# Performance work log

Measured on AMD Instinct MI355X. Metric: run time of the kernel, lower is better.

Reference implementation:

```python
import jax, jax.numpy as jnp
import numpy as np
import math

NUM_HEADS = 8
DIM_Q = 512
DIM_K = 512
DIM_V = 512
EPS = 1e-5


def _layernorm(x, g, b):
    mu = jnp.mean(x, axis=-1, keepdims=True)
    var = jnp.mean(jnp.square(x - mu), axis=-1, keepdims=True)
    return (x - mu) * jax.lax.rsqrt(var + EPS) * g + b


def setup_inputs() -> dict:
    key = jax.random.key(0)
    ks = jax.random.split(key, 16)
    B, Nq, Nk = 8, 1024, 1024
    s_q = 1.0 / math.sqrt(DIM_Q)
    s_v = 1.0 / math.sqrt(DIM_V)
    return {
        "Q": jax.random.normal(ks[0], (B, Nq, DIM_Q), jnp.float32),
        "K": jax.random.normal(ks[1], (B, Nk, DIM_K), jnp.float32),
        "Wq": jax.random.uniform(ks[2], (DIM_Q, DIM_V), jnp.float32, -s_q, s_q),
        "bq": jax.random.uniform(ks[3], (DIM_V,), jnp.float32, -s_q, s_q),
        "Wk": jax.random.uniform(ks[4], (DIM_K, DIM_V), jnp.float32, -s_q, s_q),
        "bk": jax.random.uniform(ks[5], (DIM_V,), jnp.float32, -s_q, s_q),
        "Wv": jax.random.uniform(ks[6], (DIM_K, DIM_V), jnp.float32, -s_q, s_q),
        "bv": jax.random.uniform(ks[7], (DIM_V,), jnp.float32, -s_q, s_q),
        "Wo": jax.random.uniform(ks[8], (DIM_V, DIM_V), jnp.float32, -s_v, s_v),
        "bo": jax.random.uniform(ks[9], (DIM_V,), jnp.float32, -s_v, s_v),
        "g0": jnp.ones((DIM_V,), jnp.float32),
        "b0": jnp.zeros((DIM_V,), jnp.float32),
        "g1": jnp.ones((DIM_V,), jnp.float32),
        "b1": jnp.zeros((DIM_V,), jnp.float32),
        "M": jax.random.randint(ks[10], (B, Nq, Nk), 0, 2, jnp.int32),
    }


def reference(Q, K, Wq, bq, Wk, bk, Wv, bv, Wo, bo, g0, b0, g1, b1, M):
    B, Nq, _ = Q.shape
    Nk = K.shape[1]
    H = NUM_HEADS
    d = DIM_V // H
    # projections
    Qp = Q @ Wq + bq                      # [B,Nq,Dv]
    Kp = K @ Wk + bk                      # [B,Nk,Dv]
    Vp = K @ Wv + bv                      # [B,Nk,Dv]
    # split heads: channel h*d+j -> head h (matches torch split/cat ordering)
    Qh = Qp.reshape(B, Nq, H, d)
    Kh = Kp.reshape(B, Nk, H, d)
    Vh = Vp.reshape(B, Nk, H, d)
    # scores scaled by sqrt(dim_V) (faithful to original, NOT sqrt(head_dim))
    A = jnp.einsum("bqhd,bkhd->bhqk", Qh, Kh) / math.sqrt(DIM_V)
    A = jnp.where(M[:, None, :, :] == 0, -jnp.inf, A)
    A = jax.nn.softmax(A, axis=-1)
    # residual add of the (projected, per-head) query, then merge heads
    O = Qh + jnp.einsum("bhqk,bkhd->bqhd", A, Vh)
    O = O.reshape(B, Nq, DIM_V)
    O = _layernorm(O, g0, b0)
    O = O + jax.nn.relu(O @ Wo + bo)
    O = _layernorm(O, g1, b1)
    return O
```

## Files before the change

### kernel.cpp

```cpp
#include <hip/hip_runtime.h>

typedef unsigned short u16;
typedef unsigned int u32;
typedef unsigned long long u64;
typedef __attribute__((ext_vector_type(8))) short short8;
typedef __attribute__((ext_vector_type(4))) float f32x4;
typedef __attribute__((ext_vector_type(4))) u32 u32x4;

#define BATCH 8
#define NSEQ 1024
#define DMODEL 512
#define HDIM 64
#define SCALE_LOG2E 0.06375871114929199f
#define FIXED_MAX 16.0f

#define O_QBF 0ULL
#define O_KBF 8388608ULL
#define O_WB  16777216ULL
#define O_MB  18874368ULL
#define O_QP  19922944ULL
#define O_KP  28311552ULL
#define O_VP  36700160ULL

__device__ __forceinline__ u16 f2bf(float f) {
  u32 u = __float_as_uint(f);
  u = (u + 0x7fffu + ((u >> 16) & 1u)) >> 16;
  return (u16)u;
}
__device__ __forceinline__ float bf2f(u16 s) {
  return __uint_as_float(((u32)s) << 16);
}
__device__ __forceinline__ void gload16(const void* g, void* l) {
  __builtin_amdgcn_global_load_lds((const __attribute__((address_space(1))) void*)g,
                                   (__attribute__((address_space(3))) void*)l, 16, 0, 0);
}
__device__ __forceinline__ u32 cvtpk(float a, float b) {
  u32 r;
  asm("v_cvt_pk_bf16_f32 %0, %1, %2" : "=v"(r) : "v"(a), "v"(b));
  return r;
}

__global__ __launch_bounds__(256) void prep_kernel(
    const float* __restrict__ Wq, const float* __restrict__ Wk,
    const float* __restrict__ Wv, const float* __restrict__ Wo,
    const int* __restrict__ M,
    u16* __restrict__ Wb, u64* __restrict__ Mb)
{
  __shared__ float lds[64 * 68];
  const int bi = blockIdx.x, t = threadIdx.x;
  if (bi < 256) {
    const int w = bi >> 6;
    const int tt = bi & 63;
    const int tr = tt >> 3, tc = tt & 7;
    const float* W = (w == 0) ? Wq : (w == 1) ? Wk : (w == 2) ? Wv : Wo;
#pragma unroll
    for (int j = 0; j < 4; ++j) {
      int vi = j * 256 + t;
      int row = vi >> 4, c4 = vi & 15;
      float4 v = *(const float4*)(W + (size_t)(tr * 64 + row) * 512 + tc * 64 + c4 * 4);
      lds[row * 68 + c4 * 4 + 0] = v.x;
      lds[row * 68 + c4 * 4 + 1] = v.y;
      lds[row * 68 + c4 * 4 + 2] = v.z;
      lds[row * 68 + c4 * 4 + 3] = v.w;
    }
    __syncthreads();
#pragma unroll
    for (int j = 0; j < 2; ++j) {
      int oi = j * 256 + t;
      int nl = oi >> 3, k8 = oi & 7;
      short8 o;
#pragma unroll
      for (int i = 0; i < 8; ++i) o[i] = (short)f2bf(lds[(k8 * 8 + i) * 68 + nl]);
      *(short8*)(Wb + (size_t)w * 262144 + (size_t)(tc * 64 + nl) * 512 + tr * 64 + k8 * 8) = o;
    }
  } else {
    const int pb = bi - 256;
    const int wv = t >> 6, lane = t & 63;
    for (int i = 0; i < 32; ++i) {
      int widx = pb * 128 + wv * 32 + i;
      int kc = widx & 15;
      int qq = (widx >> 4) & 1023;
      int bb = widx >> 14;
      int mv = M[((size_t)bb * 1024 + qq) * 1024 + kc * 64 + lane];
      u64 bal = __ballot(mv != 0);
      if (lane == 0) Mb[widx] = bal;
    }
  }
}

template<int MODE>
__global__ __launch_bounds__(256) void gemm_bt(
    const float* __restrict__ Fq, const float* __restrict__ Fk,
    const u16* __restrict__ Abf,
    const u16* __restrict__ Wb,
    const float* __restrict__ b0, const float* __restrict__ b1, const float* __restrict__ b2,
    u16* __restrict__ outp, const u16* __restrict__ resid)
{
  __shared__ __align__(16) char Alds[8192];
  __shared__ __align__(16) char Blds[8192];
  const int tid = threadIdx.x;
  const int wv = tid >> 6, lane = tid & 63;
  const int g16 = lane >> 4, l16 = lane & 15;
  const int wr = wv >> 1, wc = wv & 1;

  const int p = blockIdx.x;
  const int xcd = p & 7, rest = p >> 3;
  const int bx = xcd + ((rest & 7) << 3);
  const int q2 = rest >> 3;
  const int by = (MODE == 0) ? (q2 & 3) : q2;
  const int bz = (MODE == 0) ? (q2 >> 2) : 0;

  const float* Af; const u16* A; const u16* W; const float* bias; u16* out;
  if (MODE == 0) {
    Af = (bz == 0) ? Fq : Fk;
    A = nullptr;
    W = Wb + (size_t)bz * 262144;
    bias = (bz == 0) ? b0 : ((bz == 1) ? b1 : b2);
    out = outp + (size_t)bz * 4194304;
  } else {
    Af = nullptr; A = Abf; W = Wb; bias = b0; out = outp;
  }

  const int m0 = bx * 128, n0 = by * 128;
  f32x4 acc[4][4] = {};

  for (int kt = 0; kt < 16; ++kt) {
    const int k0 = kt * 32;
#pragma unroll
    for (int r = 0; r < 2; ++r) {
      int idx = r * 256 + tid;
      int row = idx >> 2, sl = idx & 3;
      if (MODE == 0) {
        const float* ap = Af + (size_t)(m0 + row) * 512 + k0 + sl * 8;
        float4 a0 = *(const float4*)(ap);
        float4 a1 = *(const float4*)(ap + 4);
        u32x4 wpk;
        wpk[0] = cvtpk(a0.x, a0.y);
        wpk[1] = cvtpk(a0.z, a0.w);
        wpk[2] = cvtpk(a1.x, a1.y);
        wpk[3] = cvtpk(a1.z, a1.w);
        *(u32x4*)(Alds + (size_t)idx * 16) = wpk;
      } else {
        gload16(A + (size_t)(m0 + row) * 512 + k0 + sl * 8, Alds + r * 4096 + wv * 1024);
      }
      gload16(W + (size_t)(n0 + row) * 512 + k0 + sl * 8, Blds + r * 4096 + wv * 1024);
    }
    __syncthreads();
    short8 af[4], bfr[4];
#pragma unroll
    for (int mt = 0; mt < 4; ++mt)
      af[mt] = *(const short8*)(Alds + (wr * 64 + mt * 16 + l16) * 64 + g16 * 16);
#pragma unroll
    for (int nt = 0; nt < 4; ++nt)
      bfr[nt] = *(const short8*)(Blds + (wc * 64 + nt * 16 + l16) * 64 + g16 * 16);
#pragma unroll
    for (int mt = 0; mt < 4; ++mt)
#pragma unroll
      for (int nt = 0; nt < 4; ++nt)
        acc[mt][nt] = __builtin_amdgcn_mfma_f32_16x16x32_bf16(af[mt], bfr[nt], acc[mt][nt], 0, 0, 0);
    __syncthreads();
  }

#pragma unroll
  for (int nt = 0; nt < 4; ++nt) {
    int col = n0 + wc * 64 + nt * 16 + l16;
    float bcol = bias[col];
#pragma unroll
    for (int mt = 0; mt < 4; ++mt) {
#pragma unroll
      for (int r = 0; r < 4; ++r) {
        int row = m0 + wr * 64 + mt * 16 + g16 * 4 + r;
        float v = acc[mt][nt][r] + bcol;
        if (MODE == 1) {
          v = fmaxf(v, 0.f) + bf2f(resid[(size_t)row * 512 + col]);
        }
        out[(size_t)row * 512 + col] = f2bf(v);
      }
    }
  }
}

__global__ __launch_bounds__(256, 4) void attn_kernel(
    const u16* __restrict__ Qp, const u16* __restrict__ Kp, const u16* __restrict__ Vp,
    const u64* __restrict__ Mb, u16* __restrict__ O1)
{
  __shared__ __align__(16) char K_lds[2][8192];
  __shared__ __align__(16) char VT_lds[2][8192];

  const int tid = threadIdx.x;
  const int wv = tid >> 6, lane = tid & 63;
  const int g16 = lane >> 4, l16 = lane & 15;
  const int l7 = l16 & 7;

  const int wg = blockIdx.x;
  const int swz = (wg & 7) * 128 + (wg >> 3);
  const int qt = swz & 15;
  const int h = (swz >> 4) & 7;
  const int b = swz >> 7;
  const int qg = qt * 64;
  const int hb = h * HDIM;
  const size_t batch_row = (size_t)b * NSEQ;

  const int q = qg + wv * 16 + l16;
  const int dv2 = (tid & 31) * 2;
  const int kg = tid >> 5;
  const int v_kc = kg >> 2, v_gg = kg & 3;

  short8 b_q[2];
#pragma unroll
  for (int c = 0; c < 2; ++c) {
    short8 raw = *(const short8*)(Qp + (batch_row + q) * DMODEL + hb + c * 32 + g16 * 8);
    short8 sc;
#pragma unroll
    for (int j = 0; j < 8; ++j) sc[j] = (short)f2bf(bf2f((u16)raw[j]) * SCALE_LOG2E);
    b_q[c] = sc;
  }

  const u64* Mq = Mb + (batch_row + q) * 16;

  auto stageK = [&](int kt2, char* dst) {
#pragma unroll
    for (int r = 0; r < 2; ++r) {
      int idx = r * 256 + tid;
      int row = idx >> 3, sl = idx & 7;
      int chunk = sl ^ (row & 7);
      gload16(Kp + (batch_row + kt2 * 64 + row) * DMODEL + hb + chunk * 8,
              dst + r * 4096 + wv * 1024);
    }
  };
  auto loadV = [&](int kt2, u32 (&vr)[8]) {
#pragma unroll
    for (int j = 0; j < 8; ++j) {
      int row = v_kc * 32 + (j >> 2) * 16 + v_gg * 4 + (j & 3);
      vr[j] = *(const u32*)(Vp + (batch_row + kt2 * 64 + row) * DMODEL + hb + dv2);
    }
  };
  auto writeVT = [&](const u32 (&vr)[8], char* dstv) {
    u32x4 lo, hi;
#pragma unroll
    for (int i = 0; i < 4; ++i) {
      lo[i] = __builtin_amdgcn_perm(vr[2 * i + 1], vr[2 * i], 0x05040100u);
      hi[i] = __builtin_amdgcn_perm(vr[2 * i + 1], vr[2 * i], 0x07060302u);
    }
    *(u32x4*)(dstv + dv2 * 128 + ((kg ^ (dv2 & 7)) << 4)) = lo;
    *(u32x4*)(dstv + (dv2 + 1) * 128 + ((kg ^ ((dv2 + 1) & 7)) << 4)) = hi;
  };

  float lL = 0.f;
  f32x4 accO[4] = {};

  u32 vreg[8];
  u64 mksA, mksB;

  stageK(0, &K_lds[0][0]);
  loadV(0, vreg);
  mksA = Mq[0];
  writeVT(vreg, &VT_lds[0][0]);
  loadV(1, vreg);

#define ATTN_TILE(KT, CUR, MKS, MKSN)                                          \
  do {                                                                         \
    asm volatile("s_waitcnt vmcnt(8) lgkmcnt(0)" ::: "memory");                \
    __builtin_amdgcn_sched_barrier(0);                                         \
    __builtin_amdgcn_s_barrier();                                              \
    __builtin_amdgcn_sched_barrier(0);                                         \
    char* Kc = &K_lds[CUR][0];                                                 \
    char* Vc = &VT_lds[CUR][0];                                                \
    if ((KT) < 15) {                                                           \
      writeVT(vreg, &VT_lds[(CUR) ^ 1][0]);                                    \
      stageK((KT) + 1, &K_lds[(CUR) ^ 1][0]);                                  \
      loadV((KT) + 2 < 16 ? (KT) + 2 : 15, vreg);                              \
      MKSN = Mq[(KT) + 1];                                                     \
    }                                                                          \
    f32x4 s_[4];                                                               \
    __builtin_amdgcn_s_setprio(1);                                             \
    _Pragma("unroll")                                                          \
    for (int kf = 0; kf < 4; ++kf) {                                           \
      int row = kf * 16 + l16;                                                 \
      short8 ak0 = *(const short8*)(Kc + row * 128 + ((g16 ^ l7) << 4));       \
      short8 ak1 = *(const short8*)(Kc + row * 128 + (((4 + g16) ^ l7) << 4)); \
      u32 nib = ((u32)((MKS) >> (kf * 16 + g16 * 4))) & 15u;                   \
      f32x4 acc;                                                               \
      acc[0] = (nib & 1u) ? 0.f : -32768.f;                                    \
      acc[1] = (nib & 2u) ? 0.f : -32768.f;                                    \
      acc[2] = (nib & 4u) ? 0.f : -32768.f;                                    \
      acc[3] = (nib & 8u) ? 0.f : -32768.f;                                    \
      acc = __builtin_amdgcn_mfma_f32_16x16x32_bf16(ak0, b_q[0], acc, 0, 0, 0);\
      acc = __builtin_amdgcn_mfma_f32_16x16x32_bf16(ak1, b_q[1], acc, 0, 0, 0);\
      s_[kf] = acc;                                                            \
    }                                                                          \
    __builtin_amdgcn_s_setprio(0);                                             \
    float sum = 0.f;                                                           \
    u32 c0a[4], c1a[4];                                                        \
    _Pragma("unroll")                                                          \
    for (int kf = 0; kf < 4; ++kf) {                                           \
      float e0 = __builtin_amdgcn_exp2f(s_[kf][0] - FIXED_MAX);                \
      float e1 = __builtin_amdgcn_exp2f(s_[kf][1] - FIXED_MAX);                \
      float e2 = __builtin_amdgcn_exp2f(s_[kf][2] - FIXED_MAX);                \
      float e3 = __builtin_amdgcn_exp2f(s_[kf][3] - FIXED_MAX);                \
      sum += (e0 + e1) + (e2 + e3);                                            \
      c0a[kf] = cvtpk(e0, e1);                                                 \
      c1a[kf] = cvtpk(e2, e3);                                                 \
    }                                                                          \
    lL += sum;                                                                 \
    u32x4 t0 = {c0a[0], c1a[0], c0a[1], c1a[1]};                               \
    u32x4 t1 = {c0a[2], c1a[2], c0a[3], c1a[3]};                               \
    short8 b_p0 = *(short8*)&t0;                                               \
    short8 b_p1 = *(short8*)&t1;                                               \
    __builtin_amdgcn_s_setprio(1);                                             \
    _Pragma("unroll")                                                          \
    for (int f = 0; f < 4; ++f) {                                              \
      int vrow = f * 16 + l16;                                                 \
      short8 av0 = *(const short8*)(Vc + vrow * 128 + ((g16 ^ l7) << 4));      \
      short8 av1 = *(const short8*)(Vc + vrow * 128 + (((4 + g16) ^ l7) << 4));\
      accO[f] = __builtin_amdgcn_mfma_f32_16x16x32_bf16(av0, b_p0, accO[f], 0, 0, 0); \
      accO[f] = __builtin_amdgcn_mfma_f32_16x16x32_bf16(av1, b_p1, accO[f], 0, 0, 0); \
    }                                                                          \
    __builtin_amdgcn_s_setprio(0);                                             \
  } while (0)

  for (int t = 0; t < 8; ++t) {
    ATTN_TILE(2 * t, 0, mksA, mksB);
    ATTN_TILE(2 * t + 1, 1, mksB, mksA);
  }
#undef ATTN_TILE

  float l = lL;
  l += __shfl_xor(l, 16, 64);
  l += __shfl_xor(l, 32, 64);
  float inv = 1.0f / fmaxf(l, 1e-20f);
#pragma unroll
  for (int f = 0; f < 4; ++f) {
    size_t o = (batch_row + q) * DMODEL + hb + f * 16 + g16 * 4;
    u64 qh = *(const u64*)(Qp + o);
    u64 ov = 0;
#pragma unroll
    for (int r = 0; r < 4; ++r) {
      float val = accO[f][r] * inv + bf2f((u16)(qh >> (r * 16)));
      ov |= ((u64)f2bf(val)) << (r * 16);
    }
    *(u64*)(O1 + o) = ov;
  }
}

template<int OUTF>
__global__ __launch_bounds__(256) void ln_kernel(
    const u16* __restrict__ X, const float* __restrict__ g, const float* __restrict__ bb,
    void* __restrict__ outv)
{
  const int tid = threadIdx.x;
  const int wv = tid >> 6, lane = tid & 63;
  const size_t row = (size_t)blockIdx.x * 4 + wv;
  short8 x8 = *(const short8*)(X + row * 512 + lane * 8);
  float xf[8];
  float s = 0.f, s2 = 0.f;
#pragma unroll
  for (int i = 0; i < 8; ++i) {
    xf[i] = bf2f((u16)x8[i]);
    s += xf[i];
    s2 += xf[i] * xf[i];
  }
#pragma unroll
  for (int d = 1; d < 64; d <<= 1) {
    s += __shfl_xor(s, d, 64);
    s2 += __shfl_xor(s2, d, 64);
  }
  float mu = s * (1.f / 512.f);
  float var = s2 * (1.f / 512.f) - mu * mu;
  float rs = rsqrtf(var + 1e-5f);
  float4 ga = *(const float4*)(g + lane * 8);
  float4 gb = *(const float4*)(g + lane * 8 + 4);
  float4 ba = *(const float4*)(bb + lane * 8);
  float4 bc = *(const float4*)(bb + lane * 8 + 4);
  float gv[8] = {ga.x, ga.y, ga.z, ga.w, gb.x, gb.y, gb.z, gb.w};
  float bv[8] = {ba.x, ba.y, ba.z, ba.w, bc.x, bc.y, bc.z, bc.w};
  float y[8];
#pragma unroll
  for (int i = 0; i < 8; ++i) y[i] = (xf[i] - mu) * rs * gv[i] + bv[i];
  if (OUTF) {
    float* o = (float*)outv + row * 512 + lane * 8;
    float4 o1 = {y[0], y[1], y[2], y[3]};
    float4 o2 = {y[4], y[5], y[6], y[7]};
    *(float4*)o = o1;
    *(float4*)(o + 4) = o2;
  } else {
    short8 o;
#pragma unroll
    for (int i = 0; i < 8; ++i) o[i] = (short)f2bf(y[i]);
    *(short8*)((u16*)outv + row * 512 + lane * 8) = o;
  }
}

extern "C" void kernel_launch(void* const* d_in, const int* in_sizes, int n_in,
                              void* d_out, int out_size, void* d_ws, size_t ws_size,
                              hipStream_t stream) {
  (void)in_sizes; (void)n_in; (void)out_size; (void)ws_size;
  const float* Q  = (const float*)d_in[0];
  const float* K  = (const float*)d_in[1];
  const float* Wq = (const float*)d_in[2];
  const float* bq = (const float*)d_in[3];
  const float* Wk = (const float*)d_in[4];
  const float* bk = (const float*)d_in[5];
  const float* Wv = (const float*)d_in[6];
  const float* bv = (const float*)d_in[7];
  const float* Wo = (const float*)d_in[8];
  const float* bo = (const float*)d_in[9];
  const float* g0 = (const float*)d_in[10];
  const float* b0 = (const float*)d_in[11];
  const float* g1 = (const float*)d_in[12];
  const float* b1 = (const float*)d_in[13];
  const int*   M  = (const int*)d_in[14];
  float* out = (float*)d_out;
  char* ws = (char*)d_ws;

  u16* Wb  = (u16*)(ws + O_WB);
  u64* Mb  = (u64*)(ws + O_MB);
  u16* Qp  = (u16*)(ws + O_QP);
  u16* Kp  = (u16*)(ws + O_KP);
  u16* Vp  = (u16*)(ws + O_VP);
  u16* O1  = (u16*)(ws + O_QBF);
  u16* Xn  = Qp;
  u16* Z   = (u16*)(ws + O_KBF);

  prep_kernel<<<1280, 256, 0, stream>>>(Wq, Wk, Wv, Wo, M, Wb, Mb);
  gemm_bt<0><<<768, 256, 0, stream>>>(Q, K, nullptr, Wb, bq, bk, bv, Qp, nullptr);
  attn_kernel<<<1024, 256, 0, stream>>>(Qp, Kp, Vp, Mb, O1);
  ln_kernel<0><<<2048, 256, 0, stream>>>(O1, g0, b0, (void*)Xn);
  gemm_bt<1><<<256, 256, 0, stream>>>(nullptr, nullptr, Xn, Wb + 3 * 262144, bo,
                                      nullptr, nullptr, Z, Xn);
  ln_kernel<1><<<2048, 256, 0, stream>>>(Z, g1, b1, (void*)out);
}
```

Before: 116.5 us.

## Move mask bit-packing into projection GEMM launch and software-pipeline fp32 A loads

The mask ballot-packing work moves out of the prep kernel into extra blocks of the QKV projection GEMM launch, so the prep kernel shrinks to weight conversion and the mask pass can run alongside the GEMM tiles. The MODE 0 GEMM now software-pipelines its main loop: fp32 A tiles are prefetched into registers two steps ahead, and W tiles are staged via async LDS loads, with explicit waitcnt and barriers. This is meant to hide global load latency behind the MFMA work and shorten the prep kernel's critical path. In exchange it adds register pressure and hand-placed synchronisation, and the mask blocks now compete with GEMM blocks for CUs.

```diff
diff --git a/kernel.cpp b/kernel.cpp
--- a/kernel.cpp
+++ b/kernel.cpp
@@ -43,41 +43,55 @@
 __global__ __launch_bounds__(256) void prep_kernel(
     const float* __restrict__ Wq, const float* __restrict__ Wk,
     const float* __restrict__ Wv, const float* __restrict__ Wo,
-    const int* __restrict__ M,
-    u16* __restrict__ Wb, u64* __restrict__ Mb)
+    u16* __restrict__ Wb)
 {
   __shared__ float lds[64 * 68];
   const int bi = blockIdx.x, t = threadIdx.x;
-  if (bi < 256) {
-    const int w = bi >> 6;
-    const int tt = bi & 63;
-    const int tr = tt >> 3, tc = tt & 7;
-    const float* W = (w == 0) ? Wq : (w == 1) ? Wk : (w == 2) ? Wv : Wo;
-#pragma unroll
-    for (int j = 0; j < 4; ++j) {
-      int vi = j * 256 + t;
-      int row = vi >> 4, c4 = vi & 15;
-      float4 v = *(const float4*)(W + (size_t)(tr * 64 + row) * 512 + tc * 64 + c4 * 4);
-      lds[row * 68 + c4 * 4 + 0] = v.x;
-      lds[row * 68 + c4 * 4 + 1] = v.y;
-      lds[row * 68 + c4 * 4 + 2] = v.z;
-      lds[row * 68 + c4 * 4 + 3] = v.w;
-    }
-    __syncthreads();
-#pragma unroll
-    for (int j = 0; j < 2; ++j) {
-      int oi = j * 256 + t;
-      int nl = oi >> 3, k8 = oi & 7;
-      short8 o;
-#pragma unroll
-      for (int i = 0; i < 8; ++i) o[i] = (short)f2bf(lds[(k8 * 8 + i) * 68 + nl]);
-      *(short8*)(Wb + (size_t)w * 262144 + (size_t)(tc * 64 + nl) * 512 + tr * 64 + k8 * 8) = o;
-    }
-  } else {
-    const int pb = bi - 256;
-    const int wv = t >> 6, lane = t & 63;
+  const int w = bi >> 6;
+  const int tt = bi & 63;
+  const int tr = tt >> 3, tc = tt & 7;
+  const float* W = (w == 0) ? Wq : (w == 1) ? Wk : (w == 2) ? Wv : Wo;
+#pragma unroll
+  for (int j = 0; j < 4; ++j) {
+    int vi = j * 256 + t;
+    int row = vi >> 4, c4 = vi & 15;
+    float4 v = *(const float4*)(W + (size_t)(tr * 64 + row) * 512 + tc * 64 + c4 * 4);
+    lds[row * 68 + c4 * 4 + 0] = v.x;
+    lds[row * 68 + c4 * 4 + 1] = v.y;
+    lds[row * 68 + c4 * 4 + 2] = v.z;
+    lds[row * 68 + c4 * 4 + 3] = v.w;
+  }
+  __syncthreads();
+#pragma unroll
+  for (int j = 0; j < 2; ++j) {
+    int oi = j * 256 + t;
+    int nl = oi >> 3, k8 = oi & 7;
+    short8 o;
+#pragma unroll
+    for (int i = 0; i < 8; ++i) o[i] = (short)f2bf(lds[(k8 * 8 + i) * 68 + nl]);
+    *(short8*)(Wb + (size_t)w * 262144 + (size_t)(tc * 64 + nl) * 512 + tr * 64 + k8 * 8) = o;
+  }
+}
+
+template<int MODE>
+__global__ __launch_bounds__(256) void gemm_bt(
+    const float* __restrict__ Fq, const float* __restrict__ Fk,
+    const u16* __restrict__ Abf,
+    const u16* __restrict__ Wb,
+    const float* __restrict__ b0, const float* __restrict__ b1, const float* __restrict__ b2,
+    u16* __restrict__ outp, const u16* __restrict__ resid,
+    const int* __restrict__ M, u64* __restrict__ Mb)
+{
+  __shared__ __align__(16) char Alds[8192];
+  __shared__ __align__(16) char Blds[8192];
+  const int tid = threadIdx.x;
+  const int p = blockIdx.x;
+
+  if (MODE == 0 && p >= 768) {
+    const int pb = p - 768;
+    const int wvp = tid >> 6, lane = tid & 63;
     for (int i = 0; i < 32; ++i) {
-      int widx = pb * 128 + wv * 32 + i;
+      int widx = pb * 128 + wvp * 32 + i;
       int kc = widx & 15;
       int qq = (widx >> 4) & 1023;
       int bb = widx >> 14;
@@ -85,25 +99,13 @@
       u64 bal = __ballot(mv != 0);
       if (lane == 0) Mb[widx] = bal;
     }
-  }
-}
-
-template<int MODE>
-__global__ __launch_bounds__(256) void gemm_bt(
-    const float* __restrict__ Fq, const float* __restrict__ Fk,
-    const u16* __restrict__ Abf,
-    const u16* __restrict__ Wb,
-    const float* __restrict__ b0, const float* __restrict__ b1, const float* __restrict__ b2,
-    u16* __restrict__ outp, const u16* __restrict__ resid)
-{
-  __shared__ __align__(16) char Alds[8192];
-  __shared__ __align__(16) char Blds[8192];
-  const int tid = threadIdx.x;
+    return;
+  }
+
   const int wv = tid >> 6, lane = tid & 63;
   const int g16 = lane >> 4, l16 = lane & 15;
   const int wr = wv >> 1, wc = wv & 1;
 
-  const int p = blockIdx.x;
   const int xcd = p & 7, rest = p >> 3;
   const int bx = xcd + ((rest & 7) << 3);
   const int q2 = rest >> 3;
@@ -124,41 +126,97 @@
   const int m0 = bx * 128, n0 = by * 128;
   f32x4 acc[4][4] = {};
 
-  for (int kt = 0; kt < 16; ++kt) {
-    const int k0 = kt * 32;
-#pragma unroll
-    for (int r = 0; r < 2; ++r) {
-      int idx = r * 256 + tid;
-      int row = idx >> 2, sl = idx & 3;
-      if (MODE == 0) {
-        const float* ap = Af + (size_t)(m0 + row) * 512 + k0 + sl * 8;
-        float4 a0 = *(const float4*)(ap);
-        float4 a1 = *(const float4*)(ap + 4);
-        u32x4 wpk;
-        wpk[0] = cvtpk(a0.x, a0.y);
-        wpk[1] = cvtpk(a0.z, a0.w);
-        wpk[2] = cvtpk(a1.x, a1.y);
-        wpk[3] = cvtpk(a1.z, a1.w);
-        *(u32x4*)(Alds + (size_t)idx * 16) = wpk;
-      } else {
+  if (MODE == 0) {
+    const int row0 = tid >> 2, sl0 = tid & 3;
+    const int row1 = (256 + tid) >> 2, sl1 = tid & 3;
+    float4 ar[4];
+    auto loadA = [&](int kt2) {
+      const float* a0 = Af + (size_t)(m0 + row0) * 512 + kt2 * 32 + sl0 * 8;
+      const float* a1 = Af + (size_t)(m0 + row1) * 512 + kt2 * 32 + sl1 * 8;
+      ar[0] = *(const float4*)(a0);
+      ar[1] = *(const float4*)(a0 + 4);
+      ar[2] = *(const float4*)(a1);
+      ar[3] = *(const float4*)(a1 + 4);
+    };
+    auto writeA = [&]() {
+      u32x4 w0, w1;
+      w0[0] = cvtpk(ar[0].x, ar[0].y); w0[1] = cvtpk(ar[0].z, ar[0].w);
+      w0[2] = cvtpk(ar[1].x, ar[1].y); w0[3] = cvtpk(ar[1].z, ar[1].w);
+      w1[0] = cvtpk(ar[2].x, ar[2].y); w1[1] = cvtpk(ar[2].z, ar[2].w);
+      w1[2] = cvtpk(ar[3].x, ar[3].y); w1[3] = cvtpk(ar[3].z, ar[3].w);
+      *(u32x4*)(Alds + (size_t)tid * 16) = w0;
+      *(u32x4*)(Alds + (size_t)(256 + tid) * 16) = w1;
+    };
+    auto stageW = [&](int kt2) {
+#pragma unroll
+      for (int r = 0; r < 2; ++r) {
+        int idx = r * 256 + tid;
+        int row = idx >> 2, sl = idx & 3;
+        gload16(W + (size_t)(n0 + row) * 512 + kt2 * 32 + sl * 8, Blds + r * 4096 + wv * 1024);
+      }
+    };
+
+    loadA(0);
+    stageW(0);
+    writeA();
+    loadA(1);
+
+    for (int kt = 0; kt < 16; ++kt) {
+      asm volatile("s_waitcnt vmcnt(4) lgkmcnt(0)" ::: "memory");
+      __builtin_amdgcn_sched_barrier(0);
+      __builtin_amdgcn_s_barrier();
+      __builtin_amdgcn_sched_barrier(0);
+
+      short8 af[4], bfr[4];
+#pragma unroll
+      for (int mt = 0; mt < 4; ++mt)
+        af[mt] = *(const short8*)(Alds + (wr * 64 + mt * 16 + l16) * 64 + g16 * 16);
+#pragma unroll
+      for (int nt = 0; nt < 4; ++nt)
+        bfr[nt] = *(const short8*)(Blds + (wc * 64 + nt * 16 + l16) * 64 + g16 * 16);
+#pragma unroll
+      for (int mt = 0; mt < 4; ++mt)
+#pragma unroll
+        for (int nt = 0; nt < 4; ++nt)
+          acc[mt][nt] = __builtin_amdgcn_mfma_f32_16x16x32_bf16(af[mt], bfr[nt], acc[mt][nt], 0, 0, 0);
+
+      __builtin_amdgcn_sched_barrier(0);
+      __builtin_amdgcn_s_barrier();
+      __builtin_amdgcn_sched_barrier(0);
+
+      if (kt < 15) {
+        stageW(kt + 1);
+        __builtin_amdgcn_sched_barrier(0);
+        writeA();
+        __builtin_amdgcn_sched_barrier(0);
+        loadA(kt + 2 < 16 ? kt + 2 : 15);
+      }
+    }
+  } else {
+    for (int kt = 0; kt < 16; ++kt) {
+      const int k0 = kt * 32;
+#pragma unroll
+      for (int r = 0; r < 2; ++r) {
+        int idx = r * 256 + tid;
+        int row = idx >> 2, sl = idx & 3;
         gload16(A + (size_t)(m0 + row) * 512 + k0 + sl * 8, Alds + r * 4096 + wv * 1024);
+        gload16(W + (size_t)(n0 + row) * 512 + k0 + sl * 8, Blds + r * 4096 + wv * 1024);
       }
-      gload16(W + (size_t)(n0 + row) * 512 + k0 + sl * 8, Blds + r * 4096 + wv * 1024);
-    }
-    __syncthreads();
-    short8 af[4], bfr[4];
-#pragma unroll
-    for (int mt = 0; mt < 4; ++mt)
-      af[mt] = *(const short8*)(Alds + (wr * 64 + mt * 16 + l16) * 64 + g16 * 16);
-#pragma unroll
-    for (int nt = 0; nt < 4; ++nt)
-      bfr[nt] = *(const short8*)(Blds + (wc * 64 + nt * 16 + l16) * 64 + g16 * 16);
-#pragma unroll
-    for (int mt = 0; mt < 4; ++mt)
+      __syncthreads();
+      short8 af[4], bfr[4];
+#pragma unroll
+      for (int mt = 0; mt < 4; ++mt)
+        af[mt] = *(const short8*)(Alds + (wr * 64 + mt * 16 + l16) * 64 + g16 * 16);
 #pragma unroll
       for (int nt = 0; nt < 4; ++nt)
-        acc[mt][nt] = __builtin_amdgcn_mfma_f32_16x16x32_bf16(af[mt], bfr[nt], acc[mt][nt], 0, 0, 0);
-    __syncthreads();
+        bfr[nt] = *(const short8*)(Blds + (wc * 64 + nt * 16 + l16) * 64 + g16 * 16);
+#pragma unroll
+      for (int mt = 0; mt < 4; ++mt)
+#pragma unroll
+        for (int nt = 0; nt < 4; ++nt)
+          acc[mt][nt] = __builtin_amdgcn_mfma_f32_16x16x32_bf16(af[mt], bfr[nt], acc[mt][nt], 0, 0, 0);
+      __syncthreads();
+    }
   }
 
 #pragma unroll
@@ -422,11 +480,11 @@
   u16* Xn  = Qp;
   u16* Z   = (u16*)(ws + O_KBF);
 
-  prep_kernel<<<1280, 256, 0, stream>>>(Wq, Wk, Wv, Wo, M, Wb, Mb);
-  gemm_bt<0><<<768, 256, 0, stream>>>(Q, K, nullptr, Wb, bq, bk, bv, Qp, nullptr);
+  prep_kernel<<<256, 256, 0, stream>>>(Wq, Wk, Wv, Wo, Wb);
+  gemm_bt<0><<<1792, 256, 0, stream>>>(Q, K, nullptr, Wb, bq, bk, bv, Qp, nullptr, M, Mb);
   attn_kernel<<<1024, 256, 0, stream>>>(Qp, Kp, Vp, Mb, O1);
   ln_kernel<0><<<2048, 256, 0, stream>>>(O1, g0, b0, (void*)Xn);
   gemm_bt<1><<<256, 256, 0, stream>>>(nullptr, nullptr, Xn, Wb + 3 * 262144, bo,
-                                      nullptr, nullptr, Z, Xn);
+                                      nullptr, nullptr, Z, Xn, nullptr, nullptr);
   ln_kernel<1><<<2048, 256, 0, stream>>>(Z, g1, b1, (void*)out);
 }
```

Result: no change. 115.5 us (-0.9%).
